# Kernel tuning notes

Hardware: AMD Instinct MI355X
Metric: run time of the kernel (lower is better)

The kernel has to match this reference:

```python
import jax, jax.numpy as jnp
import numpy as np

N, D, H, OUT, L = 4096, 127, 128, 3, 2
SIM_THRESH = 0.9
BN_EPS = 1e-5


def setup_inputs() -> dict:
    key = jax.random.key(0)
    ks = jax.random.split(key, 10)
    s = 1.0 / np.sqrt(H)
    x_now = jax.random.normal(ks[0], (N, D), dtype=jnp.float32)
    sat_type = jax.random.randint(ks[1], (N,), 0, 6, dtype=jnp.int64)
    # SAGEConv per layer: lin_l (neighbor aggr, with bias) and lin_r (root, no bias)
    Wl = jax.random.normal(ks[2], (L, H, H), dtype=jnp.float32) * s
    bl = jnp.zeros((L, H), dtype=jnp.float32)
    Wr = jax.random.normal(ks[3], (L, H, H), dtype=jnp.float32) * s
    gamma = jnp.ones((H,), dtype=jnp.float32)
    beta = jnp.zeros((H,), dtype=jnp.float32)
    Wo = jax.random.normal(ks[4], (OUT, H), dtype=jnp.float32) * s
    bo = jnp.zeros((OUT,), dtype=jnp.float32)
    return {"x_now": x_now, "sat_type": sat_type, "Wl": Wl, "bl": bl,
            "Wr": Wr, "gamma": gamma, "beta": beta, "Wo": Wo, "bo": bo}


def _forward(x_now, sat_type, Wl, bl, Wr, gamma, beta, Wo, bo):
    n = x_now.shape[0]
    # build_graph, h_prev=None branch: ppr = x_now[:, 0]
    x = jnp.concatenate([x_now[:, :1], x_now], axis=1)  # [N, H] with H = D+1
    # pairwise cosine similarity on first 4 features (F.normalize, eps=1e-12)
    f = x[:, :4]
    fn = f / jnp.maximum(jnp.linalg.norm(f, axis=1, keepdims=True), 1e-12)
    cos_sim = fn @ fn.T  # [N, N]
    same = sat_type[:, None] == sat_type[None, :]
    mask = (same | (cos_sim > SIM_THRESH)) & ~jnp.eye(n, dtype=bool)
    A = mask.astype(x.dtype)  # symmetric adjacency (dense form of edge list)
    deg = jnp.maximum(A.sum(axis=1, keepdims=True), 1.0)  # mean-aggr denom; isolated -> 0
    h = x
    for l in range(L):  # SAGEConv: lin_l(mean_j x_j) + lin_r(x_i), then ReLU
        m = (A @ h) / deg
        h = jax.nn.relu(m @ Wl[l].T + bl[l] + h @ Wr[l].T)
    # BatchNorm over nodes (training-mode batch stats, biased variance)
    mu = h.mean(axis=0)
    var = h.var(axis=0)
    h = (h - mu) / jnp.sqrt(var + BN_EPS) * gamma + beta
    out = h @ Wo.T + bo
    return h, out


def reference(x_now, sat_type, Wl, bl, Wr, gamma, beta, Wo, bo):
    return _forward(x_now, sat_type, Wl, bl, Wr, gamma, beta, Wo, bo)
```

## Files before the change

kernel.cpp:

```cpp
#include <hip/hip_runtime.h>
#include <hip/hip_bf16.h>
#include <math.h>

#define NN 4096
#define DD 127
#define HH 128
#define OUTD 3
#define NTYPES 6
#define SIM_THRESH 0.9f
#define BN_EPS 1e-5f
#define MROW 4
#define NREP 8
#define GL_STRIDE 512

typedef unsigned short ushortT;
typedef __attribute__((ext_vector_type(8))) short short8;
typedef __attribute__((ext_vector_type(4))) float f32x4;

static __device__ inline ushortT f2bf(float f) {
    unsigned u = __float_as_uint(f);
    unsigned r = (u + 0x7fffu + ((u >> 16) & 1u)) >> 16;
    return (ushortT)r;
}
static __device__ inline float bf2f(ushortT b) {
    return __uint_as_float(((unsigned)b) << 16);
}

__global__ __launch_bounds__(256) void prep(
    const float* __restrict__ x_now, const int* __restrict__ sat,
    const float* __restrict__ Wl, const float* __restrict__ Wr,
    ushortT* __restrict__ Wbf, ushortT* __restrict__ xbf,
    float4* __restrict__ fn, int* __restrict__ cnt,
    float* __restrict__ S0rep)
{
    int t = threadIdx.x;
    if (blockIdx.x < 8) {
        int baseidx = blockIdx.x * 8192;
        #pragma unroll
        for (int it = 0; it < 32; ++it) {
            int idx = baseidx + it * 256 + t;
            float v = (idx < 32768) ? Wl[idx] : Wr[idx - 32768];
            Wbf[idx] = f2bf(v);
        }
        return;
    }

    int sb = blockIdx.x - 8;
    int base = sb * 16;
    int rep = sb & (NREP - 1);
    __shared__ int stypes[16];
    int myti = -1;
    if (t < 16) {
        int row = base + t;
        int ti = sat[row]; ti = min(max(ti, 0), NTYPES - 1);
        stypes[t] = ti; myti = ti;
        const float* rp = x_now + (size_t)row * DD;
        float f0 = rp[0], f2 = rp[1], f3 = rp[2];
        float nrm = fmaxf(sqrtf(2.f * f0 * f0 + f2 * f2 + f3 * f3), 1e-12f);
        float inv = 1.f / nrm;
        fn[row] = make_float4(f0 * inv, f0 * inv, f2 * inv, f3 * inv);
    }
    #pragma unroll
    for (int it = 0; it < 8; ++it) {
        int lin = it * 256 + t;
        int rl = lin >> 7, col = lin & 127;
        int row = base + rl;
        const float* rp = x_now + (size_t)row * DD;
        float v = (col == 0) ? rp[0] : rp[col - 1];
        xbf[(size_t)row * HH + col] = f2bf(v);
    }
    __syncthreads();
    if (t < 64) {
        #pragma unroll
        for (int tt = 0; tt < NTYPES; ++tt) {
            unsigned long long m = __ballot(myti == tt);
            if (t == 0) {
                int c = __popcll(m);
                if (c) atomicAdd(&cnt[rep * NTYPES + tt], c);
            }
        }
    }
    if (t < 128) {
        float acc[NTYPES] = {0.f, 0.f, 0.f, 0.f, 0.f, 0.f};
        for (int r = 0; r < 16; ++r) {
            float v = bf2f(xbf[(size_t)(base + r) * HH + t]);
            int tt = stypes[r];
            #pragma unroll
            for (int q = 0; q < NTYPES; ++q) acc[q] += (tt == q) ? v : 0.f;
        }
        #pragma unroll
        for (int q = 0; q < NTYPES; ++q)
            atomicAdd(&S0rep[(rep * NTYPES + q) * HH + t], acc[q]);
    }
}

__global__ __launch_bounds__(256) void build_mask(
    const float4* __restrict__ fn, const int* __restrict__ sat,
    const int* __restrict__ cnt, ushortT* __restrict__ Glist,
    int* __restrict__ ncross, float* __restrict__ deg)
{
    int i0 = blockIdx.x * MROW;
    int t = threadIdx.x;
    int w = t & 127;
    int half = t >> 7;
    float4 fi[MROW];
    int ti[MROW];
    #pragma unroll
    for (int r = 0; r < MROW; ++r) {
        fi[r] = fn[i0 + r];
        int tt = sat[i0 + r];
        ti[r] = min(max(tt, 0), NTYPES - 1);
    }
    unsigned word[MROW] = {0, 0, 0, 0};
    int bbase = half * 16;
    for (int bb = 0; bb < 16; ++bb) {
        int b = bbase + bb;
        int j = b * 128 + w;
        float4 fj = fn[j];
        int tj = sat[j];
        #pragma unroll
        for (int r = 0; r < MROW; ++r) {
            float dot = fi[r].x * fj.x + fi[r].y * fj.y
                      + fi[r].z * fj.z + fi[r].w * fj.w;
            if (tj != ti[r] && dot > SIM_THRESH) word[r] |= (1u << b);
        }
    }
    __shared__ unsigned wpart[MROW][128];
    if (half == 1) {
        #pragma unroll
        for (int r = 0; r < MROW; ++r) wpart[r][w] = word[r];
    }
    __syncthreads();
    __shared__ int wt[2][MROW];
    unsigned full[MROW];
    int pcs[MROW], xin[MROW];
    int lane = w & 63, wv2 = w >> 6;
    if (half == 0) {
        #pragma unroll
        for (int r = 0; r < MROW; ++r) {
            full[r] = word[r] | wpart[r][w];
            pcs[r] = __popc(full[r]);
            xin[r] = pcs[r];
        }
        for (int s = 1; s < 64; s <<= 1) {
            #pragma unroll
            for (int r = 0; r < MROW; ++r) {
                int v = __shfl_up(xin[r], s);
                if (lane >= s) xin[r] += v;
            }
        }
        if (lane == 63) {
            #pragma unroll
            for (int r = 0; r < MROW; ++r) wt[wv2][r] = xin[r];
        }
    }
    __syncthreads();
    if (half == 0) {
        #pragma unroll
        for (int r = 0; r < MROW; ++r) {
            int excl = xin[r] - pcs[r] + (wv2 ? wt[0][r] : 0);
            int ofs = (i0 + r) * GL_STRIDE + excl;
            unsigned ww = full[r];
            while (ww) {
                int b = __ffs(ww) - 1; ww &= ww - 1;
                Glist[ofs++] = (ushortT)(b * 128 + w);
            }
        }
    }
    if (t < MROW) {
        int r = t;
        int total = wt[0][r] + wt[1][r];
        ncross[i0 + r] = total;
        int ctot = 0;
        #pragma unroll
        for (int rr = 0; rr < NREP; ++rr) ctot += cnt[rr * NTYPES + ti[r]];
        deg[i0 + r] = fmaxf((float)(ctot - 1 + total), 1.0f);
    }
}

__global__ __launch_bounds__(256, 8) void gather_kernel(
    const ushortT* __restrict__ hbf, const ushortT* __restrict__ Glist,
    const int* __restrict__ ncross, const float* __restrict__ deg,
    const float* __restrict__ S, const int* __restrict__ sat,
    ushortT* __restrict__ mbf)
{
    int t = threadIdx.x;
    int wv = t >> 6, lane = t & 63;
    int r = wv >> 1, hf = wv & 1;
    int i0 = blockIdx.x * 2;
    int i = i0 + r;

    __shared__ ushortT idx[4][256];
    __shared__ __align__(16) float part[4][HH];
    __shared__ int tarr[2];

    if (t < 2) {
        int tt = sat[i0 + t];
        tarr[t] = min(max(tt, 0), NTYPES - 1);
    }

    int n = ncross[i];
    int hcnt = (n + 1) >> 1;
    int start = hf ? hcnt : 0;
    int mycount = hf ? (n - hcnt) : hcnt;
    const ushortT* gl = Glist + (size_t)i * GL_STRIDE + start;
    #pragma unroll
    for (int b = 0; b < 4; ++b) {
        int ii = b * 64 + lane;
        if (ii < mycount) idx[wv][ii] = gl[ii];
    }

    int q = lane >> 4;
    int c = lane & 15;
    const uint4* __restrict__ hb4 = (const uint4*)hbf;
    float acc[8] = {0.f, 0.f, 0.f, 0.f, 0.f, 0.f, 0.f, 0.f};
#define BFACC(vv)                                                         \
    {                                                                     \
        acc[0] += __uint_as_float((vv).x << 16);                          \
        acc[1] += __uint_as_float((vv).x & 0xffff0000u);                  \
        acc[2] += __uint_as_float((vv).y << 16);                          \
        acc[3] += __uint_as_float((vv).y & 0xffff0000u);                  \
        acc[4] += __uint_as_float((vv).z << 16);                          \
        acc[5] += __uint_as_float((vv).z & 0xffff0000u);                  \
        acc[6] += __uint_as_float((vv).w << 16);                          \
        acc[7] += __uint_as_float((vv).w & 0xffff0000u);                  \
    }
    int g = 0;
    for (; g + 24 <= mycount; g += 24) {
        int j0 = idx[wv][g + q];
        int j1 = idx[wv][g + 4 + q];
        int j2 = idx[wv][g + 8 + q];
        int j3 = idx[wv][g + 12 + q];
        int j4 = idx[wv][g + 16 + q];
        int j5 = idx[wv][g + 20 + q];
        uint4 v0 = hb4[j0 * 16 + c];
        uint4 v1 = hb4[j1 * 16 + c];
        uint4 v2 = hb4[j2 * 16 + c];
        uint4 v3 = hb4[j3 * 16 + c];
        uint4 v4 = hb4[j4 * 16 + c];
        uint4 v5 = hb4[j5 * 16 + c];
        BFACC(v0); BFACC(v1); BFACC(v2); BFACC(v3); BFACC(v4); BFACC(v5);
    }
    for (; g + 4 <= mycount; g += 4) {
        int j0 = idx[wv][g + q];
        uint4 v0 = hb4[j0 * 16 + c];
        BFACC(v0);
    }
    if (q < mycount - g) {
        int j0 = idx[wv][g + q];
        uint4 v0 = hb4[j0 * 16 + c];
        BFACC(v0);
    }
#undef BFACC
    #pragma unroll
    for (int d = 0; d < 8; ++d) {
        acc[d] += __shfl_down(acc[d], 32);
        acc[d] += __shfl_down(acc[d], 16);
    }
    if (lane < 16) {
        float4 p0 = {acc[0], acc[1], acc[2], acc[3]};
        float4 p1 = {acc[4], acc[5], acc[6], acc[7]};
        ((float4*)part[wv])[c * 2] = p0;
        ((float4*)part[wv])[c * 2 + 1] = p1;
    }
    __syncthreads();

    if (hf == 0 && lane < 32) {
        int cc = lane;
        float4 p0 = ((const float4*)part[wv])[cc];
        float4 p1 = ((const float4*)part[wv + 1])[cc];
        int ti = tarr[r];
        float rdeg = 1.f / deg[i];
        uint2 hu = ((const uint2*)(hbf + (size_t)i * HH))[cc];
        float4 hv;
        hv.x = __uint_as_float(hu.x << 16);
        hv.y = __uint_as_float(hu.x & 0xffff0000u);
        hv.z = __uint_as_float(hu.y << 16);
        hv.w = __uint_as_float(hu.y & 0xffff0000u);
        float4 Sv = {0.f, 0.f, 0.f, 0.f};
        #pragma unroll
        for (int rr = 0; rr < NREP; ++rr) {
            float4 sv = ((const float4*)S)[(rr * NTYPES + ti) * 32 + cc];
            Sv.x += sv.x; Sv.y += sv.y; Sv.z += sv.z; Sv.w += sv.w;
        }
        float4 m;
        m.x = (Sv.x - hv.x + p0.x + p1.x) * rdeg;
        m.y = (Sv.y - hv.y + p0.y + p1.y) * rdeg;
        m.z = (Sv.z - hv.z + p0.z + p1.z) * rdeg;
        m.w = (Sv.w - hv.w + p0.w + p1.w) * rdeg;
        ushort4 mb;
        mb.x = f2bf(m.x); mb.y = f2bf(m.y);
        mb.z = f2bf(m.z); mb.w = f2bf(m.w);
        ((ushort4*)(mbf + (size_t)i * HH))[cc] = mb;
    }
}

template <int MODE>
__global__ __launch_bounds__(256) void gemm_kernel(
    const ushortT* __restrict__ mbf, const ushortT* __restrict__ hbf,
    const ushortT* __restrict__ Wlbf, const ushortT* __restrict__ Wrbf,
    const float* __restrict__ bl, const int* __restrict__ sat,
    float* __restrict__ hout, ushortT* __restrict__ houtbf,
    float* __restrict__ acc0, float* __restrict__ acc1)
{
    int t = threadIdx.x;
    int wv = t >> 6, lane = t & 63;
    int p = lane & 15, q = lane >> 4;
    int i0 = blockIdx.x * 16;

    __shared__ float sh[16][129];
    __shared__ int stypes[16];
    if (t < 16) {
        int tt = sat[i0 + t];
        stypes[t] = min(max(tt, 0), NTYPES - 1);
    }

    const ushortT* arow_m = mbf + (size_t)(i0 + p) * HH + q * 8;
    const ushortT* arow_h = hbf + (size_t)(i0 + p) * HH + q * 8;
    short8 am[4], ah[4];
    #pragma unroll
    for (int s = 0; s < 4; ++s) {
        am[s] = *(const short8*)(arow_m + s * 32);
        ah[s] = *(const short8*)(arow_h + s * 32);
    }

    #pragma unroll
    for (int nt = 0; nt < 2; ++nt) {
        int n0 = (wv * 2 + nt) * 16;
        const ushortT* brow_l = Wlbf + (size_t)(n0 + p) * HH + q * 8;
        const ushortT* brow_r = Wrbf + (size_t)(n0 + p) * HH + q * 8;
        f32x4 acc = {0.f, 0.f, 0.f, 0.f};
        #pragma unroll
        for (int s = 0; s < 4; ++s) {
            short8 b = *(const short8*)(brow_l + s * 32);
            acc = __builtin_amdgcn_mfma_f32_16x16x32_bf16(am[s], b, acc, 0, 0, 0);
        }
        #pragma unroll
        for (int s = 0; s < 4; ++s) {
            short8 b = *(const short8*)(brow_r + s * 32);
            acc = __builtin_amdgcn_mfma_f32_16x16x32_bf16(ah[s], b, acc, 0, 0, 0);
        }
        int o = n0 + p;
        float bv = bl[o];
        #pragma unroll
        for (int rg = 0; rg < 4; ++rg) {
            float v = fmaxf(acc[rg] + bv, 0.f);
            sh[q * 4 + rg][o] = v;
        }
    }
    __syncthreads();

    #pragma unroll
    for (int e = 0; e < 8; ++e) {
        int lin = e * 256 + t;
        int rr = lin >> 7, cc = lin & 127;
        float v = sh[rr][cc];
        if (MODE == 1) houtbf[(size_t)i0 * HH + lin] = f2bf(v);
        else          hout[(size_t)i0 * HH + lin] = v;
    }
    int rep = blockIdx.x & (NREP - 1);
    if (t < HH) {
        if (MODE == 1) {
            float accq[NTYPES] = {0.f, 0.f, 0.f, 0.f, 0.f, 0.f};
            for (int r = 0; r < 16; ++r) {
                float v = sh[r][t];
                int tt = stypes[r];
                #pragma unroll
                for (int qq = 0; qq < NTYPES; ++qq)
                    accq[qq] += (tt == qq) ? v : 0.f;
            }
            #pragma unroll
            for (int qq = 0; qq < NTYPES; ++qq)
                atomicAdd(&acc0[(rep * NTYPES + qq) * HH + t], accq[qq]);
        } else {
            float s = 0.f, s2 = 0.f;
            for (int r = 0; r < 16; ++r) {
                float v = sh[r][t];
                s += v; s2 += v * v;
            }
            atomicAdd(&acc0[rep * HH + t], s);
            atomicAdd(&acc1[rep * HH + t], s2);
        }
    }
}

__global__ __launch_bounds__(256) void finalize(
    const float* __restrict__ h, const float* __restrict__ musum8,
    const float* __restrict__ varsum8, const float* __restrict__ gamma,
    const float* __restrict__ beta, const float* __restrict__ Wo,
    const float* __restrict__ bo, float* __restrict__ out_h,
    float* __restrict__ out_o)
{
    int t = threadIdx.x;
    int wv = t >> 6;
    int lane = t & 63;
    int i = blockIdx.x * 4 + wv;

    float2 mus = {0.f, 0.f}, vas = {0.f, 0.f};
    #pragma unroll
    for (int r = 0; r < NREP; ++r) {
        float2 a = ((const float2*)(musum8 + r * HH))[lane];
        float2 b = ((const float2*)(varsum8 + r * HH))[lane];
        mus.x += a.x; mus.y += a.y;
        vas.x += b.x; vas.y += b.y;
    }
    float2 ga  = ((const float2*)gamma)[lane];
    float2 be  = ((const float2*)beta)[lane];
    float mu0 = mus.x * (1.f / NN), mu1 = mus.y * (1.f / NN);
    float v0 = vas.x * (1.f / NN) - mu0 * mu0;
    float v1 = vas.y * (1.f / NN) - mu1 * mu1;
    float sc0 = ga.x / sqrtf(v0 + BN_EPS), sc1 = ga.y / sqrtf(v1 + BN_EPS);
    float sh0 = be.x - mu0 * sc0, sh1 = be.y - mu1 * sc1;

    float2 hv = ((const float2*)(h + (size_t)i * HH))[lane];
    float2 hb;
    hb.x = hv.x * sc0 + sh0;
    hb.y = hv.y * sc1 + sh1;
    ((float2*)(out_h + (size_t)i * HH))[lane] = hb;

    float2 w0 = ((const float2*)Wo)[lane];
    float2 w1 = ((const float2*)(Wo + HH))[lane];
    float2 w2 = ((const float2*)(Wo + 2 * HH))[lane];
    float p0 = hb.x * w0.x + hb.y * w0.y;
    float p1 = hb.x * w1.x + hb.y * w1.y;
    float p2 = hb.x * w2.x + hb.y * w2.y;
    for (int s = 32; s; s >>= 1) {
        p0 += __shfl_down(p0, s);
        p1 += __shfl_down(p1, s);
        p2 += __shfl_down(p2, s);
    }
    if (lane == 0) {
        out_o[(size_t)i * OUTD + 0] = p0 + bo[0];
        out_o[(size_t)i * OUTD + 1] = p1 + bo[1];
        out_o[(size_t)i * OUTD + 2] = p2 + bo[2];
    }
}

extern "C" void kernel_launch(void* const* d_in, const int* in_sizes, int n_in,
                              void* d_out, int out_size, void* d_ws, size_t ws_size,
                              hipStream_t stream)
{
    (void)in_sizes; (void)n_in; (void)out_size; (void)ws_size;
    const float* x_now = (const float*)d_in[0];
    const int*   sat   = (const int*)d_in[1];
    const float* Wl    = (const float*)d_in[2];
    const float* bl    = (const float*)d_in[3];
    const float* Wr    = (const float*)d_in[4];
    const float* gamma = (const float*)d_in[5];
    const float* beta  = (const float*)d_in[6];
    const float* Wo    = (const float*)d_in[7];
    const float* bo    = (const float*)d_in[8];

    float* ws = (float*)d_ws;
    float*  h2     = ws;
    float4* fn     = (float4*)(h2 + (size_t)NN * HH);
    float*  deg    = (float*)(fn + NN);
    int*    ncross = (int*)(deg + NN);
    int*    cnt    = ncross + NN;
    float*  S0rep  = (float*)(cnt + 64);
    float*  S1rep  = S0rep + NREP * NTYPES * HH;
    float*  mu8    = S1rep + NREP * NTYPES * HH;
    float*  var8   = mu8 + NREP * HH;
    ushortT* Wbf   = (ushortT*)(var8 + NREP * HH);
    ushortT* x0bf  = Wbf + 65536;
    ushortT* h1bf  = x0bf + (size_t)NN * HH;
    ushortT* mbf   = h1bf + (size_t)NN * HH;
    ushortT* Glist = mbf + (size_t)NN * HH;

    size_t zero_bytes = (64 + 2 * NREP * NTYPES * HH + 2 * NREP * HH)
                        * sizeof(float);
    hipMemsetAsync(cnt, 0, zero_bytes, stream);

    prep<<<264, 256, 0, stream>>>(x_now, sat, Wl, Wr, Wbf, x0bf, fn, cnt,
                                  S0rep);
    build_mask<<<NN / MROW, 256, 0, stream>>>(fn, sat, cnt, Glist, ncross, deg);

    gather_kernel<<<NN / 2, 256, 0, stream>>>(x0bf, Glist, ncross, deg, S0rep,
                                              sat, mbf);
    gemm_kernel<1><<<NN / 16, 256, 0, stream>>>(
        mbf, x0bf, Wbf, Wbf + 32768, bl, sat, nullptr, h1bf, S1rep, nullptr);

    gather_kernel<<<NN / 2, 256, 0, stream>>>(h1bf, Glist, ncross, deg, S1rep,
                                              sat, mbf);
    gemm_kernel<2><<<NN / 16, 256, 0, stream>>>(
        mbf, h1bf, Wbf + 16384, Wbf + 49152, bl + HH, sat, h2, nullptr,
        mu8, var8);

    finalize<<<NN / 4, 256, 0, stream>>>(h2, mu8, var8, gamma, beta, Wo, bo,
                                         (float*)d_out, (float*)d_out + (size_t)NN * HH);
}
```

Baseline: 138.1 us.

## Replace sparse neighbor gather with dense bf16 adjacency MFMA aggregation

The build step now writes a dense bf16 0/1 matrix of cross-type similarity edges instead of compact neighbor index lists. The gather kernel is replaced by an MFMA GEMM that multiplies this matrix against a transposed feature matrix, and the prep and layer-1 GEMM kernels now also emit transposed bf16 copies of the features. This trades irregular gathers for dense tensor-core work. The cost is a 32 MB adjacency write and read per layer and N^2 compute, even though the cross-type edges are sparse.

```diff
diff --git a/kernel.cpp b/kernel.cpp
--- a/kernel.cpp
+++ b/kernel.cpp
@@ -9,9 +9,8 @@
 #define NTYPES 6
 #define SIM_THRESH 0.9f
 #define BN_EPS 1e-5f
-#define MROW 4
 #define NREP 8
-#define GL_STRIDE 512
+#define KCH 128
 
 typedef unsigned short ushortT;
 typedef __attribute__((ext_vector_type(8))) short short8;
@@ -30,8 +29,8 @@
     const float* __restrict__ x_now, const int* __restrict__ sat,
     const float* __restrict__ Wl, const float* __restrict__ Wr,
     ushortT* __restrict__ Wbf, ushortT* __restrict__ xbf,
-    float4* __restrict__ fn, int* __restrict__ cnt,
-    float* __restrict__ S0rep)
+    ushortT* __restrict__ x0T, float4* __restrict__ fn,
+    int* __restrict__ cnt, float* __restrict__ S0rep)
 {
     int t = threadIdx.x;
     if (blockIdx.x < 8) {
@@ -70,6 +69,12 @@
         xbf[(size_t)row * HH + col] = f2bf(v);
     }
     __syncthreads();
+    #pragma unroll
+    for (int it = 0; it < 8; ++it) {
+        int lin = it * 256 + t;
+        int c = lin >> 4, r = lin & 15;
+        x0T[(size_t)c * NN + base + r] = xbf[(size_t)(base + r) * HH + c];
+    }
     if (t < 64) {
         #pragma unroll
         for (int tt = 0; tt < NTYPES; ++tt) {
@@ -94,83 +99,55 @@
     }
 }
 
-__global__ __launch_bounds__(256) void build_mask(
+__global__ __launch_bounds__(256) void build_A(
     const float4* __restrict__ fn, const int* __restrict__ sat,
-    const int* __restrict__ cnt, ushortT* __restrict__ Glist,
-    int* __restrict__ ncross, float* __restrict__ deg)
-{
-    int i0 = blockIdx.x * MROW;
+    const int* __restrict__ cnt, ushortT* __restrict__ Adense,
+    float* __restrict__ deg)
+{
+    int i0 = blockIdx.x * 4;
     int t = threadIdx.x;
-    int w = t & 127;
-    int half = t >> 7;
-    float4 fi[MROW];
-    int ti[MROW];
-    #pragma unroll
-    for (int r = 0; r < MROW; ++r) {
+    float4 fi[4];
+    int ti[4];
+    #pragma unroll
+    for (int r = 0; r < 4; ++r) {
         fi[r] = fn[i0 + r];
         int tt = sat[i0 + r];
         ti[r] = min(max(tt, 0), NTYPES - 1);
     }
-    unsigned word[MROW] = {0, 0, 0, 0};
-    int bbase = half * 16;
-    for (int bb = 0; bb < 16; ++bb) {
-        int b = bbase + bb;
-        int j = b * 128 + w;
-        float4 fj = fn[j];
-        int tj = sat[j];
-        #pragma unroll
-        for (int r = 0; r < MROW; ++r) {
-            float dot = fi[r].x * fj.x + fi[r].y * fj.y
-                      + fi[r].z * fj.z + fi[r].w * fj.w;
-            if (tj != ti[r] && dot > SIM_THRESH) word[r] |= (1u << b);
-        }
-    }
-    __shared__ unsigned wpart[MROW][128];
-    if (half == 1) {
-        #pragma unroll
-        for (int r = 0; r < MROW; ++r) wpart[r][w] = word[r];
+    int cnts[4] = {0, 0, 0, 0};
+    #pragma unroll
+    for (int ch = 0; ch < 8; ++ch) {
+        int j0 = ch * 512 + t * 2;
+        float4 fa = fn[j0];
+        float4 fb = fn[j0 + 1];
+        int ta = sat[j0], tb = sat[j0 + 1];
+        #pragma unroll
+        for (int r = 0; r < 4; ++r) {
+            float da = fi[r].x * fa.x + fi[r].y * fa.y
+                     + fi[r].z * fa.z + fi[r].w * fa.w;
+            float db = fi[r].x * fb.x + fi[r].y * fb.y
+                     + fi[r].z * fb.z + fi[r].w * fb.w;
+            bool pa = (ta != ti[r]) && (da > SIM_THRESH);
+            bool pb = (tb != ti[r]) && (db > SIM_THRESH);
+            unsigned val = (pa ? 0x3F80u : 0u) | (pb ? 0x3F800000u : 0u);
+            *(unsigned*)&Adense[(size_t)(i0 + r) * NN + j0] = val;
+            cnts[r] += (int)pa + (int)pb;
+        }
+    }
+    int lane = t & 63, wv = t >> 6;
+    for (int s = 32; s; s >>= 1) {
+        #pragma unroll
+        for (int r = 0; r < 4; ++r) cnts[r] += __shfl_down(cnts[r], s);
+    }
+    __shared__ int wcnt[4][4];
+    if (lane == 0) {
+        #pragma unroll
+        for (int r = 0; r < 4; ++r) wcnt[wv][r] = cnts[r];
     }
     __syncthreads();
-    __shared__ int wt[2][MROW];
-    unsigned full[MROW];
-    int pcs[MROW], xin[MROW];
-    int lane = w & 63, wv2 = w >> 6;
-    if (half == 0) {
-        #pragma unroll
-        for (int r = 0; r < MROW; ++r) {
-            full[r] = word[r] | wpart[r][w];
-            pcs[r] = __popc(full[r]);
-            xin[r] = pcs[r];
-        }
-        for (int s = 1; s < 64; s <<= 1) {
-            #pragma unroll
-            for (int r = 0; r < MROW; ++r) {
-                int v = __shfl_up(xin[r], s);
-                if (lane >= s) xin[r] += v;
-            }
-        }
-        if (lane == 63) {
-            #pragma unroll
-            for (int r = 0; r < MROW; ++r) wt[wv2][r] = xin[r];
-        }
-    }
-    __syncthreads();
-    if (half == 0) {
-        #pragma unroll
-        for (int r = 0; r < MROW; ++r) {
-            int excl = xin[r] - pcs[r] + (wv2 ? wt[0][r] : 0);
-            int ofs = (i0 + r) * GL_STRIDE + excl;
-            unsigned ww = full[r];
-            while (ww) {
-                int b = __ffs(ww) - 1; ww &= ww - 1;
-                Glist[ofs++] = (ushortT)(b * 128 + w);
-            }
-        }
-    }
-    if (t < MROW) {
+    if (t < 4) {
         int r = t;
-        int total = wt[0][r] + wt[1][r];
-        ncross[i0 + r] = total;
+        int total = wcnt[0][r] + wcnt[1][r] + wcnt[2][r] + wcnt[3][r];
         int ctot = 0;
         #pragma unroll
         for (int rr = 0; rr < NREP; ++rr) ctot += cnt[rr * NTYPES + ti[r]];
@@ -178,120 +155,96 @@
     }
 }
 
-__global__ __launch_bounds__(256, 8) void gather_kernel(
-    const ushortT* __restrict__ hbf, const ushortT* __restrict__ Glist,
-    const int* __restrict__ ncross, const float* __restrict__ deg,
-    const float* __restrict__ S, const int* __restrict__ sat,
+__global__ __launch_bounds__(256) void agg_kernel(
+    const ushortT* __restrict__ Adense, const ushortT* __restrict__ hT,
+    const ushortT* __restrict__ hrow, const float* __restrict__ Srep,
+    const float* __restrict__ deg, const int* __restrict__ sat,
     ushortT* __restrict__ mbf)
 {
     int t = threadIdx.x;
     int wv = t >> 6, lane = t & 63;
-    int r = wv >> 1, hf = wv & 1;
-    int i0 = blockIdx.x * 2;
-    int i = i0 + r;
-
-    __shared__ ushortT idx[4][256];
-    __shared__ __align__(16) float part[4][HH];
-    __shared__ int tarr[2];
-
-    if (t < 2) {
+    int i0 = blockIdx.x * 16;
+
+    __shared__ ushortT Abuf[16][KCH + 8];
+    __shared__ ushortT Hbuf[128][KCH + 8];
+    __shared__ float esh[16][HH];
+    __shared__ float Ssum[NTYPES][HH];
+    __shared__ float rdeg[16];
+    __shared__ int ty[16];
+
+    for (int e = t; e < NTYPES * HH; e += 256) {
+        int q = e >> 7, c = e & 127;
+        float s = 0.f;
+        #pragma unroll
+        for (int rr = 0; rr < NREP; ++rr)
+            s += Srep[(rr * NTYPES + q) * HH + c];
+        Ssum[q][c] = s;
+    }
+    if (t < 16) {
+        rdeg[t] = 1.f / deg[i0 + t];
         int tt = sat[i0 + t];
-        tarr[t] = min(max(tt, 0), NTYPES - 1);
-    }
-
-    int n = ncross[i];
-    int hcnt = (n + 1) >> 1;
-    int start = hf ? hcnt : 0;
-    int mycount = hf ? (n - hcnt) : hcnt;
-    const ushortT* gl = Glist + (size_t)i * GL_STRIDE + start;
-    #pragma unroll
-    for (int b = 0; b < 4; ++b) {
-        int ii = b * 64 + lane;
-        if (ii < mycount) idx[wv][ii] = gl[ii];
-    }
-
-    int q = lane >> 4;
-    int c = lane & 15;
-    const uint4* __restrict__ hb4 = (const uint4*)hbf;
-    float acc[8] = {0.f, 0.f, 0.f, 0.f, 0.f, 0.f, 0.f, 0.f};
-#define BFACC(vv)                                                         \
-    {                                                                     \
-        acc[0] += __uint_as_float((vv).x << 16);                          \
-        acc[1] += __uint_as_float((vv).x & 0xffff0000u);                  \
-        acc[2] += __uint_as_float((vv).y << 16);                          \
-        acc[3] += __uint_as_float((vv).y & 0xffff0000u);                  \
-        acc[4] += __uint_as_float((vv).z << 16);                          \
-        acc[5] += __uint_as_float((vv).z & 0xffff0000u);                  \
-        acc[6] += __uint_as_float((vv).w << 16);                          \
-        acc[7] += __uint_as_float((vv).w & 0xffff0000u);                  \
-    }
-    int g = 0;
-    for (; g + 24 <= mycount; g += 24) {
-        int j0 = idx[wv][g + q];
-        int j1 = idx[wv][g + 4 + q];
-        int j2 = idx[wv][g + 8 + q];
-        int j3 = idx[wv][g + 12 + q];
-        int j4 = idx[wv][g + 16 + q];
-        int j5 = idx[wv][g + 20 + q];
-        uint4 v0 = hb4[j0 * 16 + c];
-        uint4 v1 = hb4[j1 * 16 + c];
-        uint4 v2 = hb4[j2 * 16 + c];
-        uint4 v3 = hb4[j3 * 16 + c];
-        uint4 v4 = hb4[j4 * 16 + c];
-        uint4 v5 = hb4[j5 * 16 + c];
-        BFACC(v0); BFACC(v1); BFACC(v2); BFACC(v3); BFACC(v4); BFACC(v5);
-    }
-    for (; g + 4 <= mycount; g += 4) {
-        int j0 = idx[wv][g + q];
-        uint4 v0 = hb4[j0 * 16 + c];
-        BFACC(v0);
-    }
-    if (q < mycount - g) {
-        int j0 = idx[wv][g + q];
-        uint4 v0 = hb4[j0 * 16 + c];
-        BFACC(v0);
-    }
-#undef BFACC
-    #pragma unroll
-    for (int d = 0; d < 8; ++d) {
-        acc[d] += __shfl_down(acc[d], 32);
-        acc[d] += __shfl_down(acc[d], 16);
-    }
-    if (lane < 16) {
-        float4 p0 = {acc[0], acc[1], acc[2], acc[3]};
-        float4 p1 = {acc[4], acc[5], acc[6], acc[7]};
-        ((float4*)part[wv])[c * 2] = p0;
-        ((float4*)part[wv])[c * 2 + 1] = p1;
+        ty[t] = min(max(tt, 0), NTYPES - 1);
+    }
+
+    int p = lane & 15, q = lane >> 4;
+    int ct0 = wv * 2, ct1 = wv * 2 + 1;
+    f32x4 acc0 = {0.f, 0.f, 0.f, 0.f};
+    f32x4 acc1 = {0.f, 0.f, 0.f, 0.f};
+
+    for (int k0 = 0; k0 < NN; k0 += KCH) {
+        {
+            int r = t >> 4, off = (t & 15) * 8;
+            *(uint4*)&Abuf[r][off] =
+                *(const uint4*)&Adense[(size_t)(i0 + r) * NN + k0 + off];
+        }
+        #pragma unroll
+        for (int rd = 0; rd < 8; ++rd) {
+            int lin = rd * 256 + t;
+            int row = lin >> 4, off = (lin & 15) * 8;
+            *(uint4*)&Hbuf[row][off] =
+                *(const uint4*)&hT[(size_t)row * NN + k0 + off];
+        }
+        __syncthreads();
+        #pragma unroll
+        for (int kk = 0; kk < KCH / 32; ++kk) {
+            short8 a  = *(const short8*)&Abuf[p][kk * 32 + q * 8];
+            short8 b0 = *(const short8*)&Hbuf[ct0 * 16 + p][kk * 32 + q * 8];
+            short8 b1 = *(const short8*)&Hbuf[ct1 * 16 + p][kk * 32 + q * 8];
+            acc0 = __builtin_amdgcn_mfma_f32_16x16x32_bf16(a, b0, acc0, 0, 0, 0);
+            acc1 = __builtin_amdgcn_mfma_f32_16x16x32_bf16(a, b1, acc1, 0, 0, 0);
+        }
+        __syncthreads();
+    }
+    #pragma unroll
+    for (int rg = 0; rg < 4; ++rg) {
+        esh[q * 4 + rg][ct0 * 16 + p] = acc0[rg];
+        esh[q * 4 + rg][ct1 * 16 + p] = acc1[rg];
     }
     __syncthreads();
 
-    if (hf == 0 && lane < 32) {
-        int cc = lane;
-        float4 p0 = ((const float4*)part[wv])[cc];
-        float4 p1 = ((const float4*)part[wv + 1])[cc];
-        int ti = tarr[r];
-        float rdeg = 1.f / deg[i];
-        uint2 hu = ((const uint2*)(hbf + (size_t)i * HH))[cc];
-        float4 hv;
-        hv.x = __uint_as_float(hu.x << 16);
-        hv.y = __uint_as_float(hu.x & 0xffff0000u);
-        hv.z = __uint_as_float(hu.y << 16);
-        hv.w = __uint_as_float(hu.y & 0xffff0000u);
-        float4 Sv = {0.f, 0.f, 0.f, 0.f};
-        #pragma unroll
-        for (int rr = 0; rr < NREP; ++rr) {
-            float4 sv = ((const float4*)S)[(rr * NTYPES + ti) * 32 + cc];
-            Sv.x += sv.x; Sv.y += sv.y; Sv.z += sv.z; Sv.w += sv.w;
-        }
-        float4 m;
-        m.x = (Sv.x - hv.x + p0.x + p1.x) * rdeg;
-        m.y = (Sv.y - hv.y + p0.y + p1.y) * rdeg;
-        m.z = (Sv.z - hv.z + p0.z + p1.z) * rdeg;
-        m.w = (Sv.w - hv.w + p0.w + p1.w) * rdeg;
-        ushort4 mb;
-        mb.x = f2bf(m.x); mb.y = f2bf(m.y);
-        mb.z = f2bf(m.z); mb.w = f2bf(m.w);
-        ((ushort4*)(mbf + (size_t)i * HH))[cc] = mb;
+    {
+        int r = t >> 4, c0 = (t & 15) * 8;
+        int i = i0 + r;
+        float rd = rdeg[r];
+        int tt = ty[r];
+        uint4 hu = *(const uint4*)&hrow[(size_t)i * HH + c0];
+        ushortT hv[8];
+        hv[0] = (ushortT)(hu.x & 0xffff); hv[1] = (ushortT)(hu.x >> 16);
+        hv[2] = (ushortT)(hu.y & 0xffff); hv[3] = (ushortT)(hu.y >> 16);
+        hv[4] = (ushortT)(hu.z & 0xffff); hv[5] = (ushortT)(hu.z >> 16);
+        hv[6] = (ushortT)(hu.w & 0xffff); hv[7] = (ushortT)(hu.w >> 16);
+        ushortT res[8];
+        #pragma unroll
+        for (int e = 0; e < 8; ++e) {
+            float m = (Ssum[tt][c0 + e] - bf2f(hv[e]) + esh[r][c0 + e]) * rd;
+            res[e] = f2bf(m);
+        }
+        uint4 w;
+        w.x = (unsigned)res[0] | ((unsigned)res[1] << 16);
+        w.y = (unsigned)res[2] | ((unsigned)res[3] << 16);
+        w.z = (unsigned)res[4] | ((unsigned)res[5] << 16);
+        w.w = (unsigned)res[6] | ((unsigned)res[7] << 16);
+        *(uint4*)&mbf[(size_t)i * HH + c0] = w;
     }
 }
 
@@ -301,6 +254,7 @@
     const ushortT* __restrict__ Wlbf, const ushortT* __restrict__ Wrbf,
     const float* __restrict__ bl, const int* __restrict__ sat,
     float* __restrict__ hout, ushortT* __restrict__ houtbf,
+    ushortT* __restrict__ houtT,
     float* __restrict__ acc0, float* __restrict__ acc1)
 {
     int t = threadIdx.x;
@@ -357,6 +311,14 @@
         float v = sh[rr][cc];
         if (MODE == 1) houtbf[(size_t)i0 * HH + lin] = f2bf(v);
         else          hout[(size_t)i0 * HH + lin] = v;
+    }
+    if (MODE == 1) {
+        #pragma unroll
+        for (int e = 0; e < 8; ++e) {
+            int lin = e * 256 + t;
+            int c = lin >> 4, r = lin & 15;
+            houtT[(size_t)c * NN + i0 + r] = f2bf(sh[r][c]);
+        }
     }
     int rep = blockIdx.x & (NREP - 1);
     if (t < HH) {
@@ -455,8 +417,7 @@
     float*  h2     = ws;
     float4* fn     = (float4*)(h2 + (size_t)NN * HH);
     float*  deg    = (float*)(fn + NN);
-    int*    ncross = (int*)(deg + NN);
-    int*    cnt    = ncross + NN;
+    int*    cnt    = (int*)(deg + NN);
     float*  S0rep  = (float*)(cnt + 64);
     float*  S1rep  = S0rep + NREP * NTYPES * HH;
     float*  mu8    = S1rep + NREP * NTYPES * HH;
@@ -465,25 +426,28 @@
     ushortT* x0bf  = Wbf + 65536;
     ushortT* h1bf  = x0bf + (size_t)NN * HH;
     ushortT* mbf   = h1bf + (size_t)NN * HH;
-    ushortT* Glist = mbf + (size_t)NN * HH;
+    ushortT* x0T   = mbf + (size_t)NN * HH;
+    ushortT* h1T   = x0T + (size_t)NN * HH;
+    ushortT* Adense = h1T + (size_t)NN * HH;
 
     size_t zero_bytes = (64 + 2 * NREP * NTYPES * HH + 2 * NREP * HH)
                         * sizeof(float);
     hipMemsetAsync(cnt, 0, zero_bytes, stream);
 
-    prep<<<264, 256, 0, stream>>>(x_now, sat, Wl, Wr, Wbf, x0bf, fn, cnt,
+    prep<<<264, 256, 0, stream>>>(x_now, sat, Wl, Wr, Wbf, x0bf, x0T, fn, cnt,
                                   S0rep);
-    build_mask<<<NN / MROW, 256, 0, stream>>>(fn, sat, cnt, Glist, ncross, deg);
-
-    gather_kernel<<<NN / 2, 256, 0, stream>>>(x0bf, Glist, ncross, deg, S0rep,
-                                              sat, mbf);
+    build_A<<<NN / 4, 256, 0, stream>>>(fn, sat, cnt, Adense, deg);
+
+    agg_kernel<<<NN / 16, 256, 0, stream>>>(Adense, x0T, x0bf, S0rep, deg, sat,
+                                            mbf);
     gemm_kernel<1><<<NN / 16, 256, 0, stream>>>(
-        mbf, x0bf, Wbf, Wbf + 32768, bl, sat, nullptr, h1bf, S1rep, nullptr);
-
-    gather_kernel<<<NN / 2, 256, 0, stream>>>(h1bf, Glist, ncross, deg, S1rep,
-                                              sat, mbf);
+        mbf, x0bf, Wbf, Wbf + 32768, bl, sat, nullptr, h1bf, h1T,
+        S1rep, nullptr);
+
+    agg_kernel<<<NN / 16, 256, 0, stream>>>(Adense, h1T, h1bf, S1rep, deg, sat,
+                                            mbf);
     gemm_kernel<2><<<NN / 16, 256, 0, stream>>>(
-        mbf, h1bf, Wbf + 16384, Wbf + 49152, bl + HH, sat, h2, nullptr,
+        mbf, h1bf, Wbf + 16384, Wbf + 49152, bl + HH, sat, h2, nullptr, nullptr,
         mu8, var8);
 
     finalize<<<NN / 4, 256, 0, stream>>>(h2, mu8, var8, gamma, beta, Wo, bo,
```

Measured after the change: 182.1 us. +31.8%, slower.
